# Kernel optimization log

Hardware: AMD Instinct MI355X
Metric: run time of the kernel (lower is better)

Reference implementation:

```python
import jax, jax.numpy as jnp
import numpy as np

B, SENSORY, UNITS, MOTOR = 4096, 64, 128, 32
ODE_UNFOLDS = 6
EPSILON = 1e-8
ELAPSED_TIME = 1.0


def setup_inputs() -> dict:
    key = jax.random.key(0)
    ks = jax.random.split(key, 16)
    u = lambda k, shape, lo, hi: jax.random.uniform(k, shape, jnp.float32, lo, hi)
    return {
        "inputs": jax.random.normal(ks[0], (B, SENSORY), jnp.float32),
        "state": jax.random.normal(ks[1], (B, UNITS), jnp.float32),
        "gleak": u(ks[2], (UNITS,), 0.001, 1.0),
        "vleak": u(ks[3], (UNITS,), -0.2, 0.2),
        "cm": u(ks[4], (UNITS,), 0.4, 0.6),
        "sigma": u(ks[5], (UNITS, UNITS), 3.0, 8.0),
        "mu": u(ks[6], (UNITS, UNITS), 0.3, 0.8),
        "w": u(ks[7], (UNITS, UNITS), 0.001, 1.0),
        "erev": jnp.sign(jax.random.normal(ks[8], (UNITS, UNITS), jnp.float32)),
        "sensory_sigma": u(ks[9], (SENSORY, UNITS), 3.0, 8.0),
        "sensory_mu": u(ks[10], (SENSORY, UNITS), 0.3, 0.8),
        "sensory_w": u(ks[11], (SENSORY, UNITS), 0.001, 1.0),
        "sensory_erev": jnp.sign(jax.random.normal(ks[12], (SENSORY, UNITS), jnp.float32)),
        "input_w": jnp.ones((SENSORY,), jnp.float32),
        "input_b": jnp.zeros((SENSORY,), jnp.float32),
        "output_w": jnp.ones((MOTOR,), jnp.float32),
        "output_b": jnp.zeros((MOTOR,), jnp.float32),
        "sparsity_mask": jax.random.randint(ks[13], (UNITS, UNITS), 0, 2) > 0,
        "sensory_sparsity_mask": jax.random.randint(ks[14], (SENSORY, UNITS), 0, 2) > 0,
    }


def reference(inputs, state, gleak, vleak, cm, sigma, mu, w, erev,
              sensory_sigma, sensory_mu, sensory_w, sensory_erev,
              input_w, input_b, output_w, output_b,
              sparsity_mask, sensory_sparsity_mask):
    mask = sparsity_mask.astype(jnp.float32)
    smask = sensory_sparsity_mask.astype(jnp.float32)

    # input mapping (affine)
    x = inputs * input_w + input_b  # [B, sensory]

    # sensory synapse activation: [B, sensory, units]
    sens_act = sensory_w * jax.nn.sigmoid(sensory_sigma * (x[:, :, None] - sensory_mu)) * smask
    w_num_sensory = jnp.sum(sens_act * sensory_erev, axis=1)  # [B, units]
    w_den_sensory = jnp.sum(sens_act, axis=1)                 # [B, units]

    cm_t = cm / (ELAPSED_TIME / ODE_UNFOLDS)  # [units]

    def step(v_pre, _):
        # [B, units, units] broadcasted synapse activation
        wa = w * jax.nn.sigmoid(sigma * (v_pre[:, :, None] - mu)) * mask
        w_num = jnp.sum(wa * erev, axis=1) + w_num_sensory
        w_den = jnp.sum(wa, axis=1) + w_den_sensory
        numerator = cm_t * v_pre + gleak * vleak + w_num
        denominator = cm_t + gleak + w_den
        return numerator / (denominator + EPSILON), None

    next_state, _ = jax.lax.scan(step, state, None, length=ODE_UNFOLDS)

    # output mapping: slice motor neurons, affine
    out = next_state[:, :MOTOR] * output_w + output_b
    return out, next_state
```

## Files before the change

### kernel.cpp

```cpp
#include <hip/hip_runtime.h>

#define BATCH    4096
#define SENS     64
#define UNITS    128
#define MOTOR_N  32
#define UNFOLDS  6
#define NB       4
#define ROWS_PER_BLOCK 16
#define NBLOCKS  (BATCH / ROWS_PER_BLOCK)

#define LOG2E 1.4426950408889634f

__device__ __forceinline__ float fast_exp2(float x) { return __builtin_amdgcn_exp2f(x); }
__device__ __forceinline__ float fast_rcp(float x)  { return __builtin_amdgcn_rcpf(x); }

__global__ __launch_bounds__(512, 2) void sensory_pre(
    const float* __restrict__ inputs,
    const float* __restrict__ gleak,  const float* __restrict__ vleak,
    const float* __restrict__ cm,
    const float* __restrict__ s_sigma, const float* __restrict__ s_mu,
    const float* __restrict__ s_w,     const float* __restrict__ s_erev,
    const float* __restrict__ input_w, const float* __restrict__ input_b,
    const int*   __restrict__ s_mask,
    float* __restrict__ num_base, float* __restrict__ den_base)
{
    __shared__ float x_lds[NB][SENS];
    __shared__ float pn[NB][4][UNITS];
    __shared__ float pd[NB][4][UNITS];

    const int t = threadIdx.x;
    const int u = t & (UNITS - 1);
    const int c = t >> 7;

    float sgL[16], smu[16], swm[16], swe[16];
#pragma unroll
    for (int k = 0; k < 16; ++k) {
        int s   = c * 16 + k;
        int idx = s * UNITS + u;
        float sig = s_sigma[idx];
        float wv  = s_w[idx] * (s_mask[idx] != 0 ? 1.0f : 0.0f);
        sgL[k] = -sig * LOG2E;
        smu[k] = s_mu[idx];
        swm[k] = wv;
        swe[k] = wv * s_erev[idx];
    }

    const int ru = u;
    const float gl  = gleak[ru];
    const float nb0 = gl * vleak[ru];
    const float db0 = cm[ru] * 6.0f + gl + 1e-8f;

    for (int g = 0; g < ROWS_PER_BLOCK / NB; ++g) {
        const int b0 = blockIdx.x * ROWS_PER_BLOCK + g * NB;

        if (t < NB * SENS) {
            int b = t >> 6, s = t & 63;
            x_lds[b][s] = inputs[(b0 + b) * SENS + s] * input_w[s] + input_b[s];
        }
        __syncthreads();

#pragma unroll 1
        for (int b = 0; b < NB; ++b) {
            float n = 0.f, d = 0.f;
            const float4* vp = (const float4*)&x_lds[b][c * 16];
#pragma unroll
            for (int q = 0; q < 4; ++q) {
                float4 v4 = vp[q];
                const float* vf = (const float*)&v4;
#pragma unroll
                for (int j = 0; j < 4; ++j) {
                    int k = q * 4 + j;
                    float e = fast_exp2(sgL[k] * (vf[j] - smu[k]));
                    float r = fast_rcp(1.0f + e);
                    n = fmaf(swe[k], r, n);
                    d = fmaf(swm[k], r, d);
                }
            }
            pn[b][c][u] = n;
            pd[b][c][u] = d;
        }
        __syncthreads();

        {
            int b = t >> 7;
            float n = pn[b][0][ru] + pn[b][1][ru] + pn[b][2][ru] + pn[b][3][ru];
            float d = pd[b][0][ru] + pd[b][1][ru] + pd[b][2][ru] + pd[b][3][ru];
            int row = b0 + b;
            num_base[row * UNITS + ru] = nb0 + n;
            den_base[row * UNITS + ru] = db0 + d;
        }
        __syncthreads();
    }
}

__global__ __launch_bounds__(1024, 4) void ltc_unfold(
    const float* __restrict__ state,
    const float* __restrict__ cm,
    const float* __restrict__ sigma, const float* __restrict__ mu,
    const float* __restrict__ w,     const float* __restrict__ erev,
    const int*   __restrict__ mask,
    const float* __restrict__ output_w, const float* __restrict__ output_b,
    const float* __restrict__ num_base, const float* __restrict__ den_base,
    float* __restrict__ out, float* __restrict__ next_state)
{
    __shared__ float v_lds[NB][UNITS];
    __shared__ float pn[NB][8][UNITS];
    __shared__ float pd[NB][8][UNITS];

    const int t = threadIdx.x;
    const int u = t & (UNITS - 1);
    const int c = t >> 7;

    float gL[16], gmu[16], gwm[16], gwe[16];
#pragma unroll
    for (int k = 0; k < 16; ++k) {
        int i   = c * 16 + k;
        int idx = i * UNITS + u;
        float sig = sigma[idx];
        float wv  = w[idx] * (mask[idx] != 0 ? 1.0f : 0.0f);
        gL[k]  = -sig * LOG2E;
        gmu[k] = mu[idx];
        gwm[k] = wv;
        gwe[k] = wv * erev[idx];
    }

    const bool red = (t < NB * UNITS);
    const int  rb  = t >> 7;
    const int  ru  = u;
    const float cmt = cm[ru] * 6.0f;

    for (int g = 0; g < ROWS_PER_BLOCK / NB; ++g) {
        const int b0 = blockIdx.x * ROWS_PER_BLOCK + g * NB;

        float vcur = 0.f, nbase = 0.f, dbase = 0.f;
        if (red) {
            int row = b0 + rb;
            vcur  = state[row * UNITS + ru];
            nbase = num_base[row * UNITS + ru];
            dbase = den_base[row * UNITS + ru];
            v_lds[rb][ru] = vcur;
        }
        __syncthreads();

#pragma unroll 1
        for (int step = 0; step < UNFOLDS; ++step) {
#pragma unroll 1
            for (int b = 0; b < NB; ++b) {
                float n = 0.f, d = 0.f;
                const float4* vp = (const float4*)&v_lds[b][c * 16];
#pragma unroll
                for (int q = 0; q < 4; ++q) {
                    float4 v4 = vp[q];
                    const float* vf = (const float*)&v4;
#pragma unroll
                    for (int j = 0; j < 4; ++j) {
                        int k = q * 4 + j;
                        float e = fast_exp2(gL[k] * (vf[j] - gmu[k]));
                        float r = fast_rcp(1.0f + e);
                        n = fmaf(gwe[k], r, n);
                        d = fmaf(gwm[k], r, d);
                    }
                }
                pn[b][c][u] = n;
                pd[b][c][u] = d;
            }
            __syncthreads();

            if (red) {
                float n = nbase, d = dbase;
#pragma unroll
                for (int cc = 0; cc < 8; ++cc) {
                    n += pn[rb][cc][ru];
                    d += pd[rb][cc][ru];
                }
                vcur = (cmt * vcur + n) * fast_rcp(d);
                v_lds[rb][ru] = vcur;
            }
            __syncthreads();
        }

        if (red) {
            int row = b0 + rb;
            next_state[row * UNITS + ru] = vcur;
            if (ru < MOTOR_N)
                out[row * MOTOR_N + ru] = vcur * output_w[ru] + output_b[ru];
        }
        __syncthreads();
    }
}

extern "C" void kernel_launch(void* const* d_in, const int* in_sizes, int n_in,
                              void* d_out, int out_size, void* d_ws, size_t ws_size,
                              hipStream_t stream) {
    const float* inputs       = (const float*)d_in[0];
    const float* state        = (const float*)d_in[1];
    const float* gleak        = (const float*)d_in[2];
    const float* vleak        = (const float*)d_in[3];
    const float* cm           = (const float*)d_in[4];
    const float* sigma        = (const float*)d_in[5];
    const float* mu           = (const float*)d_in[6];
    const float* w            = (const float*)d_in[7];
    const float* erev         = (const float*)d_in[8];
    const float* s_sigma      = (const float*)d_in[9];
    const float* s_mu         = (const float*)d_in[10];
    const float* s_w          = (const float*)d_in[11];
    const float* s_erev       = (const float*)d_in[12];
    const float* input_w      = (const float*)d_in[13];
    const float* input_b      = (const float*)d_in[14];
    const float* output_w     = (const float*)d_in[15];
    const float* output_b     = (const float*)d_in[16];
    const int*   mask         = (const int*)d_in[17];
    const int*   s_mask       = (const int*)d_in[18];

    float* out        = (float*)d_out;
    float* next_state = out + (size_t)BATCH * MOTOR_N;

    float* num_base = (float*)d_ws;
    float* den_base = num_base + (size_t)BATCH * UNITS;

    sensory_pre<<<NBLOCKS, 512, 0, stream>>>(
        inputs, gleak, vleak, cm, s_sigma, s_mu, s_w, s_erev,
        input_w, input_b, s_mask, num_base, den_base);

    ltc_unfold<<<NBLOCKS, 1024, 0, stream>>>(
        state, cm, sigma, mu, w, erev, mask,
        output_w, output_b, num_base, den_base, out, next_state);
}
```

Before: 212.0 us.

## Fuse sensory precompute into unfold kernel and simplify sigmoid arithmetic

Merges the sensory synapse precompute into the ODE unfold kernel, so the per-row sensory numerator/denominator bases are computed in shared memory instead of round-tripping through a global workspace and a second launch. The sigmoid argument is refactored into a single FMA with a precomputed bias, and the denominator weight is derived as the absolute value of the signed weight, dropping one per-synapse register array. This relies on erev being exactly ±1, and adds register pressure from holding both recurrent and sensory parameters, with asm barriers pinning them in VGPRs.

```diff
diff --git a/kernel.cpp b/kernel.cpp
--- a/kernel.cpp
+++ b/kernel.cpp
@@ -8,101 +8,27 @@
 #define NB       4
 #define ROWS_PER_BLOCK 16
 #define NBLOCKS  (BATCH / ROWS_PER_BLOCK)
+#define NGROUPS  (ROWS_PER_BLOCK / NB)
 
 #define LOG2E 1.4426950408889634f
 
 __device__ __forceinline__ float fast_exp2(float x) { return __builtin_amdgcn_exp2f(x); }
 __device__ __forceinline__ float fast_rcp(float x)  { return __builtin_amdgcn_rcpf(x); }
 
-__global__ __launch_bounds__(512, 2) void sensory_pre(
-    const float* __restrict__ inputs,
-    const float* __restrict__ gleak,  const float* __restrict__ vleak,
+__global__ __launch_bounds__(1024, 4) void ltc_fused(
+    const float* __restrict__ inputs,  const float* __restrict__ state,
+    const float* __restrict__ gleak,   const float* __restrict__ vleak,
     const float* __restrict__ cm,
+    const float* __restrict__ sigma,   const float* __restrict__ mu,
+    const float* __restrict__ w,       const float* __restrict__ erev,
     const float* __restrict__ s_sigma, const float* __restrict__ s_mu,
     const float* __restrict__ s_w,     const float* __restrict__ s_erev,
     const float* __restrict__ input_w, const float* __restrict__ input_b,
-    const int*   __restrict__ s_mask,
-    float* __restrict__ num_base, float* __restrict__ den_base)
+    const float* __restrict__ output_w,const float* __restrict__ output_b,
+    const int*   __restrict__ mask,    const int* __restrict__ s_mask,
+    float* __restrict__ out, float* __restrict__ next_state)
 {
     __shared__ float x_lds[NB][SENS];
-    __shared__ float pn[NB][4][UNITS];
-    __shared__ float pd[NB][4][UNITS];
-
-    const int t = threadIdx.x;
-    const int u = t & (UNITS - 1);
-    const int c = t >> 7;
-
-    float sgL[16], smu[16], swm[16], swe[16];
-#pragma unroll
-    for (int k = 0; k < 16; ++k) {
-        int s   = c * 16 + k;
-        int idx = s * UNITS + u;
-        float sig = s_sigma[idx];
-        float wv  = s_w[idx] * (s_mask[idx] != 0 ? 1.0f : 0.0f);
-        sgL[k] = -sig * LOG2E;
-        smu[k] = s_mu[idx];
-        swm[k] = wv;
-        swe[k] = wv * s_erev[idx];
-    }
-
-    const int ru = u;
-    const float gl  = gleak[ru];
-    const float nb0 = gl * vleak[ru];
-    const float db0 = cm[ru] * 6.0f + gl + 1e-8f;
-
-    for (int g = 0; g < ROWS_PER_BLOCK / NB; ++g) {
-        const int b0 = blockIdx.x * ROWS_PER_BLOCK + g * NB;
-
-        if (t < NB * SENS) {
-            int b = t >> 6, s = t & 63;
-            x_lds[b][s] = inputs[(b0 + b) * SENS + s] * input_w[s] + input_b[s];
-        }
-        __syncthreads();
-
-#pragma unroll 1
-        for (int b = 0; b < NB; ++b) {
-            float n = 0.f, d = 0.f;
-            const float4* vp = (const float4*)&x_lds[b][c * 16];
-#pragma unroll
-            for (int q = 0; q < 4; ++q) {
-                float4 v4 = vp[q];
-                const float* vf = (const float*)&v4;
-#pragma unroll
-                for (int j = 0; j < 4; ++j) {
-                    int k = q * 4 + j;
-                    float e = fast_exp2(sgL[k] * (vf[j] - smu[k]));
-                    float r = fast_rcp(1.0f + e);
-                    n = fmaf(swe[k], r, n);
-                    d = fmaf(swm[k], r, d);
-                }
-            }
-            pn[b][c][u] = n;
-            pd[b][c][u] = d;
-        }
-        __syncthreads();
-
-        {
-            int b = t >> 7;
-            float n = pn[b][0][ru] + pn[b][1][ru] + pn[b][2][ru] + pn[b][3][ru];
-            float d = pd[b][0][ru] + pd[b][1][ru] + pd[b][2][ru] + pd[b][3][ru];
-            int row = b0 + b;
-            num_base[row * UNITS + ru] = nb0 + n;
-            den_base[row * UNITS + ru] = db0 + d;
-        }
-        __syncthreads();
-    }
-}
-
-__global__ __launch_bounds__(1024, 4) void ltc_unfold(
-    const float* __restrict__ state,
-    const float* __restrict__ cm,
-    const float* __restrict__ sigma, const float* __restrict__ mu,
-    const float* __restrict__ w,     const float* __restrict__ erev,
-    const int*   __restrict__ mask,
-    const float* __restrict__ output_w, const float* __restrict__ output_b,
-    const float* __restrict__ num_base, const float* __restrict__ den_base,
-    float* __restrict__ out, float* __restrict__ next_state)
-{
     __shared__ float v_lds[NB][UNITS];
     __shared__ float pn[NB][8][UNITS];
     __shared__ float pd[NB][8][UNITS];
@@ -111,34 +37,80 @@
     const int u = t & (UNITS - 1);
     const int c = t >> 7;
 
-    float gL[16], gmu[16], gwm[16], gwe[16];
+    float rgl[16], rgb[16], rws[16];
 #pragma unroll
     for (int k = 0; k < 16; ++k) {
-        int i   = c * 16 + k;
-        int idx = i * UNITS + u;
-        float sig = sigma[idx];
-        float wv  = w[idx] * (mask[idx] != 0 ? 1.0f : 0.0f);
-        gL[k]  = -sig * LOG2E;
-        gmu[k] = mu[idx];
-        gwm[k] = wv;
-        gwe[k] = wv * erev[idx];
+        int idx = (c * 16 + k) * UNITS + u;
+        float sg = sigma[idx] * LOG2E;
+        float wv = w[idx] * (mask[idx] != 0 ? 1.0f : 0.0f);
+        rgl[k] = -sg;
+        rgb[k] = sg * mu[idx];
+        rws[k] = wv * erev[idx];
     }
+    float sgl[8], sgb[8], sws[8];
+#pragma unroll
+    for (int j = 0; j < 8; ++j) {
+        int idx = (c * 8 + j) * UNITS + u;
+        float sg = s_sigma[idx] * LOG2E;
+        float wv = s_w[idx] * (s_mask[idx] != 0 ? 1.0f : 0.0f);
+        sgl[j] = -sg;
+        sgb[j] = sg * s_mu[idx];
+        sws[j] = wv * s_erev[idx];
+    }
+#pragma unroll
+    for (int k = 0; k < 16; ++k)
+        asm volatile("" : "+v"(rgl[k]), "+v"(rgb[k]), "+v"(rws[k]));
+#pragma unroll
+    for (int j = 0; j < 8; ++j)
+        asm volatile("" : "+v"(sgl[j]), "+v"(sgb[j]), "+v"(sws[j]));
 
     const bool red = (t < NB * UNITS);
     const int  rb  = t >> 7;
     const int  ru  = u;
     const float cmt = cm[ru] * 6.0f;
+    const float nb0 = gleak[ru] * vleak[ru];
+    const float db0 = cmt + gleak[ru] + 1e-8f;
 
-    for (int g = 0; g < ROWS_PER_BLOCK / NB; ++g) {
+    for (int g = 0; g < NGROUPS; ++g) {
         const int b0 = blockIdx.x * ROWS_PER_BLOCK + g * NB;
 
+        if (t < NB * SENS) {
+            int b = t >> 6, s = t & 63;
+            x_lds[b][s] = inputs[(b0 + b) * SENS + s] * input_w[s] + input_b[s];
+        }
         float vcur = 0.f, nbase = 0.f, dbase = 0.f;
         if (red) {
-            int row = b0 + rb;
-            vcur  = state[row * UNITS + ru];
-            nbase = num_base[row * UNITS + ru];
-            dbase = den_base[row * UNITS + ru];
+            vcur = state[(b0 + rb) * UNITS + ru];
             v_lds[rb][ru] = vcur;
+        }
+        __syncthreads();
+
+#pragma unroll 1
+        for (int b = 0; b < NB; ++b) {
+            float n = 0.f, d = 0.f;
+            const float4* xp = (const float4*)&x_lds[b][c * 8];
+            float4 xa = xp[0], xb = xp[1];
+            float xs[8] = {xa.x, xa.y, xa.z, xa.w, xb.x, xb.y, xb.z, xb.w};
+#pragma unroll
+            for (int j = 0; j < 8; ++j) {
+                float e = fast_exp2(fmaf(sgl[j], xs[j], sgb[j]));
+                float r = fast_rcp(1.0f + e);
+                n = fmaf(sws[j], r, n);
+                d = fmaf(fabsf(sws[j]), r, d);
+            }
+            pn[b][c][u] = n;
+            pd[b][c][u] = d;
+        }
+        __syncthreads();
+
+        if (red) {
+            float n = nb0, d = db0;
+#pragma unroll
+            for (int cc = 0; cc < 8; ++cc) {
+                n += pn[rb][cc][ru];
+                d += pd[rb][cc][ru];
+            }
+            nbase = n; dbase = d;
         }
         __syncthreads();
 
@@ -153,12 +125,12 @@
                     float4 v4 = vp[q];
                     const float* vf = (const float*)&v4;
 #pragma unroll
-                    for (int j = 0; j < 4; ++j) {
-                        int k = q * 4 + j;
-                        float e = fast_exp2(gL[k] * (vf[j] - gmu[k]));
+                    for (int jj = 0; jj < 4; ++jj) {
+                        int k = q * 4 + jj;
+                        float e = fast_exp2(fmaf(rgl[k], vf[jj], rgb[k]));
                         float r = fast_rcp(1.0f + e);
-                        n = fmaf(gwe[k], r, n);
-                        d = fmaf(gwm[k], r, d);
+                        n = fmaf(rws[k], r, n);
+                        d = fmaf(fabsf(rws[k]), r, d);
                     }
                 }
                 pn[b][c][u] = n;
@@ -173,7 +145,7 @@
                     n += pn[rb][cc][ru];
                     d += pd[rb][cc][ru];
                 }
-                vcur = (cmt * vcur + n) * fast_rcp(d);
+                vcur = fmaf(cmt, vcur, n) * fast_rcp(d);
                 v_lds[rb][ru] = vcur;
             }
             __syncthreads();
@@ -192,37 +164,31 @@
 extern "C" void kernel_launch(void* const* d_in, const int* in_sizes, int n_in,
                               void* d_out, int out_size, void* d_ws, size_t ws_size,
                               hipStream_t stream) {
-    const float* inputs       = (const float*)d_in[0];
-    const float* state        = (const float*)d_in[1];
-    const float* gleak        = (const float*)d_in[2];
-    const float* vleak        = (const float*)d_in[3];
-    const float* cm           = (const float*)d_in[4];
-    const float* sigma        = (const float*)d_in[5];
-    const float* mu           = (const float*)d_in[6];
-    const float* w            = (const float*)d_in[7];
-    const float* erev         = (const float*)d_in[8];
-    const float* s_sigma      = (const float*)d_in[9];
-    const float* s_mu         = (const float*)d_in[10];
-    const float* s_w          = (const float*)d_in[11];
-    const float* s_erev       = (const float*)d_in[12];
-    const float* input_w      = (const float*)d_in[13];
-    const float* input_b      = (const float*)d_in[14];
-    const float* output_w     = (const float*)d_in[15];
-    const float* output_b     = (const float*)d_in[16];
-    const int*   mask         = (const int*)d_in[17];
-    const int*   s_mask       = (const int*)d_in[18];
+    const float* inputs   = (const float*)d_in[0];
+    const float* state    = (const float*)d_in[1];
+    const float* gleak    = (const float*)d_in[2];
+    const float* vleak    = (const float*)d_in[3];
+    const float* cm       = (const float*)d_in[4];
+    const float* sigma    = (const float*)d_in[5];
+    const float* mu       = (const float*)d_in[6];
+    const float* w        = (const float*)d_in[7];
+    const float* erev     = (const float*)d_in[8];
+    const float* s_sigma  = (const float*)d_in[9];
+    const float* s_mu     = (const float*)d_in[10];
+    const float* s_w      = (const float*)d_in[11];
+    const float* s_erev   = (const float*)d_in[12];
+    const float* input_w  = (const float*)d_in[13];
+    const float* input_b  = (const float*)d_in[14];
+    const float* output_w = (const float*)d_in[15];
+    const float* output_b = (const float*)d_in[16];
+    const int*   mask     = (const int*)d_in[17];
+    const int*   s_mask   = (const int*)d_in[18];
 
     float* out        = (float*)d_out;
     float* next_state = out + (size_t)BATCH * MOTOR_N;
 
-    float* num_base = (float*)d_ws;
-    float* den_base = num_base + (size_t)BATCH * UNITS;
-
-    sensory_pre<<<NBLOCKS, 512, 0, stream>>>(
-        inputs, gleak, vleak, cm, s_sigma, s_mu, s_w, s_erev,
-        input_w, input_b, s_mask, num_base, den_base);
-
-    ltc_unfold<<<NBLOCKS, 1024, 0, stream>>>(
-        state, cm, sigma, mu, w, erev, mask,
-        output_w, output_b, num_base, den_base, out, next_state);
+    ltc_fused<<<NBLOCKS, 1024, 0, stream>>>(
+        inputs, state, gleak, vleak, cm, sigma, mu, w, erev,
+        s_sigma, s_mu, s_w, s_erev, input_w, input_b, output_w, output_b,
+        mask, s_mask, out, next_state);
 }
```

New measurement: 199.3 us. 1.06x faster.
